# Optimization experiments

Measured on AMD Instinct MI355X. Metric: run time of the kernel, lower is better.

## Reference

```python
import jax, jax.numpy as jnp
import numpy as np

D_MODEL = 768
NUM_HEADS = 12
HEAD_DIM = D_MODEL // NUM_HEADS


def setup_inputs() -> dict:
    key = jax.random.key(0)
    ks = jax.random.split(key, 5)
    B, T = 2, 4096
    x = jax.random.normal(ks[0], (B, T, D_MODEL), dtype=jnp.float32)
    s_in = 1.0 / np.sqrt(D_MODEL)
    W_attn = jax.random.normal(ks[1], (D_MODEL, 3 * D_MODEL), dtype=jnp.float32) * s_in
    b_attn = jnp.zeros((3 * D_MODEL,), dtype=jnp.float32)
    W_proj = jax.random.normal(ks[2], (D_MODEL, D_MODEL), dtype=jnp.float32) * s_in
    b_proj = jnp.zeros((D_MODEL,), dtype=jnp.float32)
    return {"x": x, "W_attn": W_attn, "b_attn": b_attn, "W_proj": W_proj, "b_proj": b_proj}


def reference(x, W_attn, b_attn, W_proj, b_proj):
    B, T, C = x.shape
    H, D = NUM_HEADS, HEAD_DIM
    qkv = x @ W_attn + b_attn                      # [B,T,3C]
    q, k, v = jnp.split(qkv, 3, axis=-1)
    q = q.reshape(B, T, H, D).transpose(0, 2, 1, 3)  # [B,H,T,D]
    k = k.reshape(B, T, H, D).transpose(0, 2, 1, 3)
    v = v.reshape(B, T, H, D).transpose(0, 2, 1, 3)
    scores = jnp.einsum('bhqd,bhkd->bhqk', q, k) / jnp.sqrt(jnp.float32(D))
    attn = jax.nn.softmax(scores, axis=-1)          # [B,H,T,T]
    out = jnp.einsum('bhqk,bhkd->bhqd', attn, v)    # [B,H,T,D]
    out = out.transpose(0, 2, 1, 3).reshape(B, T, C)
    return out @ W_proj + b_proj
```

## Files before the change

kernel.cpp:

```cpp
#include <hip/hip_runtime.h>
#include <cstdint>
#include <cstddef>

#define DEV static __device__ __forceinline__

typedef __attribute__((ext_vector_type(8))) short bf16x8;
typedef __attribute__((ext_vector_type(4))) float f32x4;
typedef __attribute__((ext_vector_type(16))) float f32x16;

#define T_SEQ 4096
#define CDIM  768
#define NH    12
#define HD    64
#define NBH   24
#define M_ROWS 8192

#define OFF_XB   0ull
#define OFF_WAT  (OFF_XB  + (size_t)M_ROWS * CDIM * 2)
#define OFF_WPT  (OFF_WAT + (size_t)(3*CDIM) * CDIM * 2)
#define OFF_Q    (OFF_WPT + (size_t)CDIM * CDIM * 2)
#define OFF_K    (OFF_Q   + (size_t)NBH * T_SEQ * HD * 2)
#define OFF_VT   (OFF_K   + (size_t)NBH * T_SEQ * HD * 2)
#define OFF_O    (OFF_VT  + (size_t)NBH * HD * T_SEQ * 2)

DEV unsigned short f2bf(float f) {
  unsigned u = __builtin_bit_cast(unsigned, f);
  u += 0x7FFFu + ((u >> 16) & 1u);
  return (unsigned short)(u >> 16);
}

DEV void gld_lds16(const void* g, void* l) {
  __builtin_amdgcn_global_load_lds(
      (const __attribute__((address_space(1))) void*)g,
      (__attribute__((address_space(3))) void*)l, 16, 0, 0);
}

__global__ __launch_bounds__(256) void k_conv(const float* __restrict__ in,
                                              unsigned short* __restrict__ out) {
  int i = blockIdx.x * 256 + threadIdx.x;
  const float4* p = (const float4*)in;
  float4 a = p[i * 2], b = p[i * 2 + 1];
  uint4 o;
  o.x = (unsigned)f2bf(a.x) | ((unsigned)f2bf(a.y) << 16);
  o.y = (unsigned)f2bf(a.z) | ((unsigned)f2bf(a.w) << 16);
  o.z = (unsigned)f2bf(b.x) | ((unsigned)f2bf(b.y) << 16);
  o.w = (unsigned)f2bf(b.z) | ((unsigned)f2bf(b.w) << 16);
  ((uint4*)out)[i] = o;
}

__global__ __launch_bounds__(256) void k_transpose(const float* __restrict__ in,
                                                   unsigned short* __restrict__ out,
                                                   int R, int C) {
  __shared__ float tile[64][65];
  int c0 = blockIdx.x * 64, r0 = blockIdx.y * 64;
  int tid = threadIdx.x;
  for (int i = tid; i < 4096; i += 256) {
    int r = i >> 6, c = i & 63;
    tile[r][c] = in[(size_t)(r0 + r) * C + c0 + c];
  }
  __syncthreads();
  for (int i = tid; i < 4096; i += 256) {
    int c = i >> 6, r = i & 63;
    out[(size_t)(c0 + c) * R + r0 + r] = f2bf(tile[r][c]);
  }
}

__global__ __launch_bounds__(256) void k_qkv(const unsigned short* __restrict__ A,
                                             const unsigned short* __restrict__ Bt,
                                             const float* __restrict__ bias,
                                             unsigned short* __restrict__ Qo,
                                             unsigned short* __restrict__ Ko,
                                             unsigned short* __restrict__ Vt) {
  __shared__ short As[128 * 64];
  __shared__ short Bs[128 * 64];
  const int tid = threadIdx.x;
  const int wave = tid >> 6, lane = tid & 63;
  const int wr = wave >> 1, wc = wave & 1;
  const int m0 = blockIdx.y * 128, n0 = blockIdx.x * 128;

  f32x4 acc[4][4] = {};

#pragma unroll 1
  for (int k0 = 0; k0 < 768; k0 += 64) {
#pragma unroll
    for (int it = 0; it < 4; ++it) {
      int chunk = wave * 4 + it;
      int slot = chunk * 64 + lane;
      int row = slot >> 3, j = slot & 7;
      int kcol = k0 + ((j ^ (row & 7)) << 3);
      gld_lds16(A  + (size_t)(m0 + row) * 768 + kcol, &As[chunk * 512]);
      gld_lds16(Bt + (size_t)(n0 + row) * 768 + kcol, &Bs[chunk * 512]);
    }
    __syncthreads();
#pragma unroll
    for (int kk = 0; kk < 2; ++kk) {
      bf16x8 af[4], bfr[4];
      int cbl = kk * 4 + (lane >> 4);
#pragma unroll
      for (int mi = 0; mi < 4; ++mi) {
        int row = wr * 64 + mi * 16 + (lane & 15);
        af[mi] = *(const bf16x8*)&As[(row * 8 + (cbl ^ (row & 7))) * 8];
      }
#pragma unroll
      for (int ni = 0; ni < 4; ++ni) {
        int row = wc * 64 + ni * 16 + (lane & 15);
        bfr[ni] = *(const bf16x8*)&Bs[(row * 8 + (cbl ^ (row & 7))) * 8];
      }
#pragma unroll
      for (int mi = 0; mi < 4; ++mi)
#pragma unroll
        for (int ni = 0; ni < 4; ++ni)
          acc[mi][ni] = __builtin_amdgcn_mfma_f32_16x16x32_bf16(af[mi], bfr[ni], acc[mi][ni], 0, 0, 0);
    }
    __syncthreads();
  }

  const int which = n0 / 768;
#pragma unroll
  for (int ni = 0; ni < 4; ++ni) {
    int col = n0 + wc * 64 + ni * 16 + (lane & 15);
    int nr = col - which * 768;
    int h = nr >> 6, d = nr & 63;
    float bi = bias[col];
#pragma unroll
    for (int mi = 0; mi < 4; ++mi) {
      int mt = m0 + wr * 64 + mi * 16 + ((lane >> 4) << 2);
      int b = mt >> 12, t = mt & 4095;
      size_t bh = (size_t)(b * NH + h);
#pragma unroll
      for (int r = 0; r < 4; ++r) {
        float v = acc[mi][ni][r] + bi;
        if (which == 0) {
          Qo[bh * (T_SEQ * HD) + (size_t)(t + r) * HD + d] = f2bf(v * 0.18033688011112042f);
        } else if (which == 1) {
          Ko[bh * (T_SEQ * HD) + (size_t)(t + r) * HD + d] = f2bf(v);
        } else {
          int tc = t + r;
          int pc = (tc & ~12) | ((tc & 4) << 1) | ((tc & 8) >> 1);
          Vt[bh * (T_SEQ * HD) + (size_t)d * T_SEQ + pc] = f2bf(v);
        }
      }
    }
  }
}

__global__ __launch_bounds__(256, 3) void k_attn(const unsigned short* __restrict__ Q,
                                                 const unsigned short* __restrict__ K,
                                                 const unsigned short* __restrict__ Vt,
                                                 unsigned short* __restrict__ O) {
  __shared__ char ldsb[2][16384];
  const int tid = threadIdx.x, wave = tid >> 6, lane = tid & 63;
  const int hi = lane >> 5, l31 = lane & 31;
  const int qt = blockIdx.x, bh = blockIdx.y;
  const int b = bh / NH, h = bh % NH;
  const size_t base = (size_t)bh * T_SEQ * HD;
  const int q0 = qt * 128 + wave * 32;

  bf16x8 aq[4];
#pragma unroll
  for (int t = 0; t < 4; ++t)
    aq[t] = *(const bf16x8*)&Q[base + (size_t)(q0 + l31) * HD + t * 16 + hi * 8];

  int koff[4];
#pragma unroll
  for (int t = 0; t < 4; ++t)
    koff[t] = l31 * 128 + ((((t << 1) | hi) ^ (l31 & 7)) << 4);
  int voff[2][2];
#pragma unroll
  for (int kb = 0; kb < 2; ++kb)
#pragma unroll
    for (int ks = 0; ks < 2; ++ks)
      voff[kb][ks] = ((((kb << 2) | (ks << 1) | hi) ^ (l31 & 7)) << 4) + l31 * 128;

  f32x16 oacc0 = {}, oacc1 = {}, lacc = {};
  union { unsigned u[4]; bf16x8 v; } onesf;
  onesf.u[0] = 0x3F803F80u; onesf.u[1] = 0x3F803F80u;
  onesf.u[2] = 0x3F803F80u; onesf.u[3] = 0x3F803F80u;

  auto STAGE = [&](int bufi, int k0) {
#pragma unroll
    for (int it = 0; it < 2; ++it) {
      int chunk = wave * 2 + it;
      int slot = chunk * 64 + lane;
      int row = slot >> 3, j = slot & 7;
      int ce = ((j ^ (row & 7)) << 3);
      gld_lds16(K  + base + (size_t)(k0 + row) * HD + ce, ldsb[bufi] + chunk * 1024);
      gld_lds16(Vt + base + (size_t)row * T_SEQ + k0 + ce, ldsb[bufi] + 8192 + chunk * 1024);
    }
  };

  STAGE(0, 0);
  __syncthreads();

  int buf = 0;
#pragma unroll 1
  for (int kt = 0; kt < 64; ++kt) {
    if (kt < 63) STAGE(buf ^ 1, (kt + 1) * 64);
    const char* Lp = ldsb[buf];
#pragma unroll
    for (int kb = 0; kb < 2; ++kb) {
      f32x16 s = {};
      const char* Kp = Lp + kb * 4096;
#pragma unroll
      for (int t = 0; t < 4; ++t) {
        bf16x8 kf = *(const bf16x8*)(Kp + koff[t]);
        s = __builtin_amdgcn_mfma_f32_32x32x16_bf16(kf, aq[t], s, 0, 0, 0);
      }
#pragma unroll
      for (int r = 0; r < 16; ++r) s[r] = __builtin_amdgcn_exp2f(s[r]);
      unsigned w[8];
#pragma unroll
      for (int i = 0; i < 8; ++i) {
        unsigned wi;
        asm("v_cvt_pk_bf16_f32 %0, %1, %2" : "=v"(wi) : "v"(s[2 * i]), "v"(s[2 * i + 1]));
        w[i] = wi;
      }
      asm volatile("s_nop 2");
      union { unsigned u[4]; bf16x8 v; } pf0, pf1;
      pf0.u[0] = w[0]; pf0.u[1] = w[1]; pf0.u[2] = w[2]; pf0.u[3] = w[3];
      pf1.u[0] = w[4]; pf1.u[1] = w[5]; pf1.u[2] = w[6]; pf1.u[3] = w[7];
      const char* Vp = Lp + 8192;
      lacc = __builtin_amdgcn_mfma_f32_32x32x16_bf16(pf0.v, onesf.v, lacc, 0, 0, 0);
      lacc = __builtin_amdgcn_mfma_f32_32x32x16_bf16(pf1.v, onesf.v, lacc, 0, 0, 0);
#pragma unroll
      for (int ks = 0; ks < 2; ++ks) {
        bf16x8 v0 = *(const bf16x8*)(Vp + voff[kb][ks]);
        bf16x8 v1 = *(const bf16x8*)(Vp + 4096 + voff[kb][ks]);
        oacc0 = __builtin_amdgcn_mfma_f32_32x32x16_bf16(ks ? pf1.v : pf0.v, v0, oacc0, 0, 0, 0);
        oacc1 = __builtin_amdgcn_mfma_f32_32x32x16_bf16(ks ? pf1.v : pf0.v, v1, oacc1, 0, 0, 0);
      }
    }
    __syncthreads();
    buf ^= 1;
  }

#pragma unroll
  for (int r = 0; r < 16; ++r) {
    float inv = 1.0f / lacc[r];
    int t = q0 + ((r & 3) + 8 * (r >> 2)) + 4 * hi;
    size_t rowb = (size_t)(b * T_SEQ + t) * CDIM + h * 64;
    O[rowb + l31]      = f2bf(oacc0[r] * inv);
    O[rowb + 32 + l31] = f2bf(oacc1[r] * inv);
  }
}

__global__ __launch_bounds__(256) void k_proj(const unsigned short* __restrict__ A,
                                              const unsigned short* __restrict__ Bt,
                                              const float* __restrict__ bias,
                                              float* __restrict__ out) {
  __shared__ short As[128 * 64];
  __shared__ short Bs[128 * 64];
  const int tid = threadIdx.x;
  const int wave = tid >> 6, lane = tid & 63;
  const int wr = wave >> 1, wc = wave & 1;
  const int m0 = blockIdx.y * 128, n0 = blockIdx.x * 128;

  f32x4 acc[4][4] = {};

#pragma unroll 1
  for (int k0 = 0; k0 < 768; k0 += 64) {
#pragma unroll
    for (int it = 0; it < 4; ++it) {
      int chunk = wave * 4 + it;
      int slot = chunk * 64 + lane;
      int row = slot >> 3, j = slot & 7;
      int kcol = k0 + ((j ^ (row & 7)) << 3);
      gld_lds16(A  + (size_t)(m0 + row) * 768 + kcol, &As[chunk * 512]);
      gld_lds16(Bt + (size_t)(n0 + row) * 768 + kcol, &Bs[chunk * 512]);
    }
    __syncthreads();
#pragma unroll
    for (int kk = 0; kk < 2; ++kk) {
      bf16x8 af[4], bfr[4];
      int cbl = kk * 4 + (lane >> 4);
#pragma unroll
      for (int mi = 0; mi < 4; ++mi) {
        int row = wr * 64 + mi * 16 + (lane & 15);
        af[mi] = *(const bf16x8*)&As[(row * 8 + (cbl ^ (row & 7))) * 8];
      }
#pragma unroll
      for (int ni = 0; ni < 4; ++ni) {
        int row = wc * 64 + ni * 16 + (lane & 15);
        bfr[ni] = *(const bf16x8*)&Bs[(row * 8 + (cbl ^ (row & 7))) * 8];
      }
#pragma unroll
      for (int mi = 0; mi < 4; ++mi)
#pragma unroll
        for (int ni = 0; ni < 4; ++ni)
          acc[mi][ni] = __builtin_amdgcn_mfma_f32_16x16x32_bf16(af[mi], bfr[ni], acc[mi][ni], 0, 0, 0);
    }
    __syncthreads();
  }

#pragma unroll
  for (int ni = 0; ni < 4; ++ni) {
    int col = n0 + wc * 64 + ni * 16 + (lane & 15);
    float bi = bias[col];
#pragma unroll
    for (int mi = 0; mi < 4; ++mi) {
      int mt = m0 + wr * 64 + mi * 16 + ((lane >> 4) << 2);
#pragma unroll
      for (int r = 0; r < 4; ++r)
        out[(size_t)(mt + r) * CDIM + col] = acc[mi][ni][r] + bi;
    }
  }
}

extern "C" void kernel_launch(void* const* d_in, const int* in_sizes, int n_in,
                              void* d_out, int out_size, void* d_ws, size_t ws_size,
                              hipStream_t stream) {
  const float* x  = (const float*)d_in[0];
  const float* Wa = (const float*)d_in[1];
  const float* ba = (const float*)d_in[2];
  const float* Wp = (const float*)d_in[3];
  const float* bp = (const float*)d_in[4];

  char* ws = (char*)d_ws;
  unsigned short* xb  = (unsigned short*)(ws + OFF_XB);
  unsigned short* WaT = (unsigned short*)(ws + OFF_WAT);
  unsigned short* WpT = (unsigned short*)(ws + OFF_WPT);
  unsigned short* Qb  = (unsigned short*)(ws + OFF_Q);
  unsigned short* Kb  = (unsigned short*)(ws + OFF_K);
  unsigned short* Vtb = (unsigned short*)(ws + OFF_VT);
  unsigned short* Ob  = (unsigned short*)(ws + OFF_O);

  k_conv<<<3072, 256, 0, stream>>>(x, xb);
  k_transpose<<<dim3(36, 12), 256, 0, stream>>>(Wa, WaT, CDIM, 3 * CDIM);
  k_transpose<<<dim3(12, 12), 256, 0, stream>>>(Wp, WpT, CDIM, CDIM);
  k_qkv<<<dim3(18, 64), 256, 0, stream>>>(xb, WaT, ba, Qb, Kb, Vtb);
  k_attn<<<dim3(32, 24), 256, 0, stream>>>(Qb, Kb, Vtb, Ob);
  k_proj<<<dim3(6, 64), 256, 0, stream>>>(Ob, WpT, bp, (float*)d_out);
}
```

Measured before the change: 229.6 us.

## Split attention KV range across two blocks and add combine kernel

Splits the attention key dimension into two halves via a third grid dimension, so each block processes 32 KV tiles instead of 64. Each half writes unnormalized bf16 partial outputs and row sums, and a new combine kernel adds the halves and normalizes. This doubles the block count (768 to 1536) to better fill the 256 CUs, and raises the occupancy hint to 4 blocks per CU. In exchange it adds a partial-output round trip through memory, an extra launch, and extra bf16 rounding of the unnormalized partials. Summing the halves without a max correction is valid because the kernel already applies exp2 with no running max.

```diff
diff --git a/kernel.cpp b/kernel.cpp
--- a/kernel.cpp
+++ b/kernel.cpp
@@ -22,11 +22,18 @@
 #define OFF_K    (OFF_Q   + (size_t)NBH * T_SEQ * HD * 2)
 #define OFF_VT   (OFF_K   + (size_t)NBH * T_SEQ * HD * 2)
 #define OFF_O    (OFF_VT  + (size_t)NBH * HD * T_SEQ * 2)
+#define OFF_P    (OFF_O   + (size_t)M_ROWS * CDIM * 2)
+#define OFF_L    (OFF_P   + 2ull * M_ROWS * CDIM * 2)
 
 DEV unsigned short f2bf(float f) {
   unsigned u = __builtin_bit_cast(unsigned, f);
   u += 0x7FFFu + ((u >> 16) & 1u);
   return (unsigned short)(u >> 16);
+}
+
+DEV float bf2f(unsigned short s) {
+  unsigned u = (unsigned)s << 16;
+  return __builtin_bit_cast(float, u);
 }
 
 DEV void gld_lds16(const void* g, void* l) {
@@ -144,14 +151,15 @@
   }
 }
 
-__global__ __launch_bounds__(256, 3) void k_attn(const unsigned short* __restrict__ Q,
+__global__ __launch_bounds__(256, 4) void k_attn(const unsigned short* __restrict__ Q,
                                                  const unsigned short* __restrict__ K,
                                                  const unsigned short* __restrict__ Vt,
-                                                 unsigned short* __restrict__ O) {
+                                                 unsigned short* __restrict__ Op,
+                                                 float* __restrict__ Lp) {
   __shared__ char ldsb[2][16384];
   const int tid = threadIdx.x, wave = tid >> 6, lane = tid & 63;
   const int hi = lane >> 5, l31 = lane & 31;
-  const int qt = blockIdx.x, bh = blockIdx.y;
+  const int qt = blockIdx.x, bh = blockIdx.y, ks = blockIdx.z;
   const int b = bh / NH, h = bh % NH;
   const size_t base = (size_t)bh * T_SEQ * HD;
   const int q0 = qt * 128 + wave * 32;
@@ -169,8 +177,8 @@
 #pragma unroll
   for (int kb = 0; kb < 2; ++kb)
 #pragma unroll
-    for (int ks = 0; ks < 2; ++ks)
-      voff[kb][ks] = ((((kb << 2) | (ks << 1) | hi) ^ (l31 & 7)) << 4) + l31 * 128;
+    for (int kss = 0; kss < 2; ++kss)
+      voff[kb][kss] = ((((kb << 2) | (kss << 1) | hi) ^ (l31 & 7)) << 4) + l31 * 128;
 
   f32x16 oacc0 = {}, oacc1 = {}, lacc = {};
   union { unsigned u[4]; bf16x8 v; } onesf;
@@ -189,18 +197,19 @@
     }
   };
 
-  STAGE(0, 0);
+  const int kt0 = ks * 32, ktEnd = kt0 + 32;
+  STAGE(0, kt0 * 64);
   __syncthreads();
 
   int buf = 0;
 #pragma unroll 1
-  for (int kt = 0; kt < 64; ++kt) {
-    if (kt < 63) STAGE(buf ^ 1, (kt + 1) * 64);
-    const char* Lp = ldsb[buf];
+  for (int kt = kt0; kt < ktEnd; ++kt) {
+    if (kt + 1 < ktEnd) STAGE(buf ^ 1, (kt + 1) * 64);
+    const char* Lq = ldsb[buf];
 #pragma unroll
     for (int kb = 0; kb < 2; ++kb) {
       f32x16 s = {};
-      const char* Kp = Lp + kb * 4096;
+      const char* Kp = Lq + kb * 4096;
 #pragma unroll
       for (int t = 0; t < 4; ++t) {
         bf16x8 kf = *(const bf16x8*)(Kp + koff[t]);
@@ -219,29 +228,61 @@
       union { unsigned u[4]; bf16x8 v; } pf0, pf1;
       pf0.u[0] = w[0]; pf0.u[1] = w[1]; pf0.u[2] = w[2]; pf0.u[3] = w[3];
       pf1.u[0] = w[4]; pf1.u[1] = w[5]; pf1.u[2] = w[6]; pf1.u[3] = w[7];
-      const char* Vp = Lp + 8192;
+      const char* Vp = Lq + 8192;
       lacc = __builtin_amdgcn_mfma_f32_32x32x16_bf16(pf0.v, onesf.v, lacc, 0, 0, 0);
       lacc = __builtin_amdgcn_mfma_f32_32x32x16_bf16(pf1.v, onesf.v, lacc, 0, 0, 0);
 #pragma unroll
-      for (int ks = 0; ks < 2; ++ks) {
-        bf16x8 v0 = *(const bf16x8*)(Vp + voff[kb][ks]);
-        bf16x8 v1 = *(const bf16x8*)(Vp + 4096 + voff[kb][ks]);
-        oacc0 = __builtin_amdgcn_mfma_f32_32x32x16_bf16(ks ? pf1.v : pf0.v, v0, oacc0, 0, 0, 0);
-        oacc1 = __builtin_amdgcn_mfma_f32_32x32x16_bf16(ks ? pf1.v : pf0.v, v1, oacc1, 0, 0, 0);
+      for (int kss = 0; kss < 2; ++kss) {
+        bf16x8 v0 = *(const bf16x8*)(Vp + voff[kb][kss]);
+        bf16x8 v1 = *(const bf16x8*)(Vp + 4096 + voff[kb][kss]);
+        oacc0 = __builtin_amdgcn_mfma_f32_32x32x16_bf16(kss ? pf1.v : pf0.v, v0, oacc0, 0, 0, 0);
+        oacc1 = __builtin_amdgcn_mfma_f32_32x32x16_bf16(kss ? pf1.v : pf0.v, v1, oacc1, 0, 0, 0);
       }
     }
     __syncthreads();
     buf ^= 1;
   }
 
+  unsigned short* OpS = Op + (size_t)ks * M_ROWS * CDIM;
+  float* LpS = Lp + (size_t)ks * NBH * T_SEQ;
 #pragma unroll
   for (int r = 0; r < 16; ++r) {
-    float inv = 1.0f / lacc[r];
     int t = q0 + ((r & 3) + 8 * (r >> 2)) + 4 * hi;
     size_t rowb = (size_t)(b * T_SEQ + t) * CDIM + h * 64;
-    O[rowb + l31]      = f2bf(oacc0[r] * inv);
-    O[rowb + 32 + l31] = f2bf(oacc1[r] * inv);
-  }
+    OpS[rowb + l31]      = f2bf(oacc0[r]);
+    OpS[rowb + 32 + l31] = f2bf(oacc1[r]);
+    if (l31 == 0) LpS[(size_t)bh * T_SEQ + t] = lacc[r];
+  }
+}
+
+__global__ __launch_bounds__(256) void k_combine(const unsigned short* __restrict__ Op,
+                                                 const float* __restrict__ Lp,
+                                                 unsigned short* __restrict__ Ob) {
+  int i = blockIdx.x * 256 + threadIdx.x;
+  size_t e = (size_t)i * 8;
+  int c = (int)(e % CDIM);
+  int bt = (int)(e / CDIM);
+  int t = bt & 4095, b = bt >> 12;
+  int h = c >> 6;
+  size_t li = (size_t)(b * NH + h) * T_SEQ + t;
+  float inv = 1.0f / (Lp[li] + Lp[(size_t)NBH * T_SEQ + li]);
+  uint4 p0 = ((const uint4*)Op)[i];
+  uint4 p1 = ((const uint4*)(Op + (size_t)M_ROWS * CDIM))[i];
+  unsigned pw0[4] = {p0.x, p0.y, p0.z, p0.w};
+  unsigned pw1[4] = {p1.x, p1.y, p1.z, p1.w};
+  unsigned ow[4];
+#pragma unroll
+  for (int k = 0; k < 4; ++k) {
+    float a0 = __builtin_bit_cast(float, pw0[k] << 16);
+    float a1 = __builtin_bit_cast(float, pw0[k] & 0xFFFF0000u);
+    float b0 = __builtin_bit_cast(float, pw1[k] << 16);
+    float b1 = __builtin_bit_cast(float, pw1[k] & 0xFFFF0000u);
+    unsigned short lo = f2bf((a0 + b0) * inv);
+    unsigned short hiw = f2bf((a1 + b1) * inv);
+    ow[k] = (unsigned)lo | ((unsigned)hiw << 16);
+  }
+  uint4 o; o.x = ow[0]; o.y = ow[1]; o.z = ow[2]; o.w = ow[3];
+  ((uint4*)Ob)[i] = o;
 }
 
 __global__ __launch_bounds__(256) void k_proj(const unsigned short* __restrict__ A,
@@ -323,11 +364,14 @@
   unsigned short* Kb  = (unsigned short*)(ws + OFF_K);
   unsigned short* Vtb = (unsigned short*)(ws + OFF_VT);
   unsigned short* Ob  = (unsigned short*)(ws + OFF_O);
+  unsigned short* Opb = (unsigned short*)(ws + OFF_P);
+  float*          Lpb = (float*)(ws + OFF_L);
 
   k_conv<<<3072, 256, 0, stream>>>(x, xb);
   k_transpose<<<dim3(36, 12), 256, 0, stream>>>(Wa, WaT, CDIM, 3 * CDIM);
   k_transpose<<<dim3(12, 12), 256, 0, stream>>>(Wp, WpT, CDIM, CDIM);
   k_qkv<<<dim3(18, 64), 256, 0, stream>>>(xb, WaT, ba, Qb, Kb, Vtb);
-  k_attn<<<dim3(32, 24), 256, 0, stream>>>(Qb, Kb, Vtb, Ob);
+  k_attn<<<dim3(32, 24, 2), 256, 0, stream>>>(Qb, Kb, Vtb, Opb, Lpb);
+  k_combine<<<3072, 256, 0, stream>>>(Opb, Lpb, Ob);
   k_proj<<<dim3(6, 64), 256, 0, stream>>>(Ob, WpT, bp, (float*)d_out);
 }
```

Measured after the change: 239.5 us. 4.3% more time.
